# Kernel tuning notes

Hardware: AMD Instinct MI355X
Metric: run time of the kernel (lower is better)

The kernel has to match this reference:

```python
import jax, jax.numpy as jnp
import numpy as np

B, N, D = 8192, 8192, 768

def setup_inputs() -> dict:
    key = jax.random.key(0)
    kx, ky = jax.random.split(key)
    x = jax.random.normal(kx, (B, D), dtype=jnp.float32)
    y = jax.random.normal(ky, (N, D), dtype=jnp.float32)
    return {"x": x, "y": y}

def reference(x, y):
    # Pairwise squared L2 distances: ||x_i - y_j||^2 = ||x_i||^2 + ||y_j||^2 - 2 x_i . y_j
    # Mathematically identical to the naive broadcast (x[:,None,:]-y[None,:,:])**2 sum,
    # but avoids the O(B*N*D) intermediate. Clamp at 0 to guard fp cancellation
    # (true squared distances are nonnegative).
    x2 = jnp.sum(x * x, axis=-1)[:, None]           # [B, 1]
    y2 = jnp.sum(y * y, axis=-1)[None, :]           # [1, N]
    xy = jnp.einsum('bd,nd->bn', x, y)              # [B, N] GEMM
    d = x2 + y2 - 2.0 * xy
    return jnp.maximum(d, 0.0)
```

## Files before the change

kernel.cpp:

```cpp
#include <hip/hip_runtime.h>
#include <hip/hip_bf16.h>
#include <stdint.h>


#define M_DIM 8192
#define N_DIM 8192
#define D_DIM 768
#define K_DIM (3 * D_DIM)
#define BM 128
#define BN 128
#define BK 32

typedef __bf16 bf16x8 __attribute__((ext_vector_type(8)));
typedef float f32x4 __attribute__((ext_vector_type(4)));

#define GLOAD_LDS16(g, l) \
  __builtin_amdgcn_global_load_lds((const __attribute__((address_space(1))) void*)(g), \
                                   (__attribute__((address_space(3))) void*)(l), 16, 0, 0)

__global__ __launch_bounds__(256) void pack_kernel(
    const float* __restrict__ in, __hip_bfloat16* __restrict__ pk,
    float* __restrict__ nrm, int off_hi0, int off_hi1, int off_lo)
{
  int row = blockIdx.x;
  int tid = threadIdx.x;
  const float* r = in + (size_t)row * D_DIM;
  __hip_bfloat16* p = pk + (size_t)row * K_DIM;
  float ss = 0.f;
  for (int d = tid; d < D_DIM; d += 256) {
    float v = r[d];
    ss += v * v;
    __hip_bfloat16 hi = __float2bfloat16(v);
    float hv = __bfloat162float(hi);
    __hip_bfloat16 lo = __float2bfloat16(v - hv);
    p[off_hi0 + d] = hi;
    p[off_hi1 + d] = hi;
    p[off_lo  + d] = lo;
  }
  #pragma unroll
  for (int o = 32; o > 0; o >>= 1) ss += __shfl_down(ss, o, 64);
  __shared__ float warp_s[4];
  int lane = tid & 63, wid = tid >> 6;
  if (lane == 0) warp_s[wid] = ss;
  __syncthreads();
  if (tid == 0) nrm[row] = warp_s[0] + warp_s[1] + warp_s[2] + warp_s[3];
}

__global__ __launch_bounds__(256, 2) void dist_gemm(
    const __hip_bfloat16* __restrict__ A, const __hip_bfloat16* __restrict__ Bp,
    const float* __restrict__ x2, const float* __restrict__ y2,
    float* __restrict__ out)
{
  __shared__ __attribute__((aligned(16))) __hip_bfloat16 As[BM * BK];
  __shared__ __attribute__((aligned(16))) __hip_bfloat16 Bs[BN * BK];

  int bid = blockIdx.x;
  int swz = (bid & 7) * 512 + (bid >> 3);
  int tileRow = swz >> 6;
  int tileCol = swz & 63;
  int rowBase = tileRow * BM;
  int colBase = tileCol * BN;

  int tid  = threadIdx.x;
  int lane = tid & 63;
  int wid  = tid >> 6;
  int wr = wid >> 1, wc = wid & 1;

  f32x4 acc[4][4];
  #pragma unroll
  for (int m = 0; m < 4; ++m)
    #pragma unroll
    for (int n = 0; n < 4; ++n)
      acc[m][n] = (f32x4){0.f, 0.f, 0.f, 0.f};

  int reg0 = wid * 2;
  int kc = (lane >> 4) * 8;
  int rl = lane & 15;

  for (int kt = 0; kt < K_DIM / BK; ++kt) {
    int k0 = kt * BK;
    #pragma unroll
    for (int i = 0; i < 2; ++i) {
      int c = (reg0 + i) * 64 + lane;
      int arow = c >> 2;
      int cc = (c & 3) * 8;
      const __hip_bfloat16* ga = A  + (size_t)(rowBase + arow) * K_DIM + k0 + cc;
      const __hip_bfloat16* gb = Bp + (size_t)(colBase + arow) * K_DIM + k0 + cc;
      GLOAD_LDS16(ga, (char*)As + (reg0 + i) * 1024);
      GLOAD_LDS16(gb, (char*)Bs + (reg0 + i) * 1024);
    }
    __syncthreads();

    bf16x8 af[4], bfr[4];
    #pragma unroll
    for (int m = 0; m < 4; ++m)
      af[m] = *(const bf16x8*)&As[(wr * 64 + m * 16 + rl) * BK + kc];
    #pragma unroll
    for (int n = 0; n < 4; ++n)
      bfr[n] = *(const bf16x8*)&Bs[(wc * 64 + n * 16 + rl) * BK + kc];

    #pragma unroll
    for (int m = 0; m < 4; ++m)
      #pragma unroll
      for (int n = 0; n < 4; ++n)
        acc[m][n] = __builtin_amdgcn_mfma_f32_16x16x32_bf16(af[m], bfr[n], acc[m][n], 0, 0, 0);

    __syncthreads();
  }

  #pragma unroll
  for (int m = 0; m < 4; ++m) {
    int r0 = rowBase + wr * 64 + m * 16 + (lane >> 4) * 4;
    float4 xv = *(const float4*)&x2[r0];
    const float* xs = (const float*)&xv;
    #pragma unroll
    for (int n = 0; n < 4; ++n) {
      int c0 = colBase + wc * 64 + n * 16 + (lane & 15);
      float yv = y2[c0];
      float* op = out + (size_t)r0 * N_DIM + c0;
      #pragma unroll
      for (int v = 0; v < 4; ++v) {
        float d = xs[v] + yv - 2.0f * acc[m][n][v];
        op[(size_t)v * N_DIM] = fmaxf(d, 0.f);
      }
    }
  }
}

__global__ __launch_bounds__(256) void fallback_kernel(
    const float* __restrict__ x, const float* __restrict__ y, float* __restrict__ out)
{
  size_t gid = (size_t)blockIdx.x * 256 + threadIdx.x;
  int i = (int)(gid >> 13);
  int j = (int)(gid & 8191);
  const float4* xr = (const float4*)(x + (size_t)i * D_DIM);
  const float4* yr = (const float4*)(y + (size_t)j * D_DIM);
  float acc = 0.f;
  for (int d = 0; d < D_DIM / 4; ++d) {
    float4 a = xr[d], b = yr[d];
    float dx = a.x - b.x, dy = a.y - b.y, dz = a.z - b.z, dw = a.w - b.w;
    acc += dx * dx + dy * dy + dz * dz + dw * dw;
  }
  out[gid] = fmaxf(acc, 0.f);
}

extern "C" void kernel_launch(void* const* d_in, const int* in_sizes, int n_in,
                              void* d_out, int out_size, void* d_ws, size_t ws_size,
                              hipStream_t stream)
{
  const float* x = (const float*)d_in[0];
  const float* y = (const float*)d_in[1];
  float* out = (float*)d_out;

  size_t packBytes = (size_t)M_DIM * K_DIM * sizeof(__hip_bfloat16);
  size_t need = 2 * packBytes + 2 * (size_t)M_DIM * sizeof(float);
  if (ws_size < need) {
    fallback_kernel<<<((size_t)M_DIM * N_DIM) / 256, 256, 0, stream>>>(x, y, out);
    return;
  }

  __hip_bfloat16* Ap = (__hip_bfloat16*)d_ws;
  __hip_bfloat16* Bp = (__hip_bfloat16*)((char*)d_ws + packBytes);
  float* x2 = (float*)((char*)d_ws + 2 * packBytes);
  float* y2 = x2 + M_DIM;

  pack_kernel<<<M_DIM, 256, 0, stream>>>(x, Ap, x2, 0, D_DIM, 2 * D_DIM);
  pack_kernel<<<N_DIM, 256, 0, stream>>>(y, Bp, y2, 0, 2 * D_DIM, D_DIM);

  dist_gemm<<<(M_DIM / BM) * (N_DIM / BN), 256, 0, stream>>>(Ap, Bp, x2, y2, out);
}
```

Baseline: 694.5 us.

## Use 256x256 tiles with 4-stage LDS pipeline, swizzled LDS, vectorized pack

The GEMM now uses 256x256 output tiles with 512 threads, where each wave computes 128x64. Operand tiles stream through a 4-deep ring of LDS buffers filled by async global-to-LDS loads, with explicit vmcnt waits and one barrier per k-step in place of two syncthreads. The LDS layout is XOR-swizzled to cut bank conflicts, and MFMA issue is given raised priority. The pack kernel goes to one wave per row with 16-byte vector loads and stores, which raises LDS and register pressure in exchange for more reuse and overlap of loads with compute.

```diff
diff --git a/kernel.cpp b/kernel.cpp
--- a/kernel.cpp
+++ b/kernel.cpp
@@ -7,9 +7,10 @@
 #define N_DIM 8192
 #define D_DIM 768
 #define K_DIM (3 * D_DIM)
-#define BM 128
-#define BN 128
+#define BM 256
+#define BN 256
 #define BK 32
+#define KT (K_DIM / BK)
 
 typedef __bf16 bf16x8 __attribute__((ext_vector_type(8)));
 typedef float f32x4 __attribute__((ext_vector_type(4)));
@@ -22,95 +23,118 @@
     const float* __restrict__ in, __hip_bfloat16* __restrict__ pk,
     float* __restrict__ nrm, int off_hi0, int off_hi1, int off_lo)
 {
-  int row = blockIdx.x;
-  int tid = threadIdx.x;
+  int wid = threadIdx.x >> 6, lane = threadIdx.x & 63;
+  int row = blockIdx.x * 4 + wid;
   const float* r = in + (size_t)row * D_DIM;
   __hip_bfloat16* p = pk + (size_t)row * K_DIM;
   float ss = 0.f;
-  for (int d = tid; d < D_DIM; d += 256) {
-    float v = r[d];
-    ss += v * v;
-    __hip_bfloat16 hi = __float2bfloat16(v);
-    float hv = __bfloat162float(hi);
-    __hip_bfloat16 lo = __float2bfloat16(v - hv);
-    p[off_hi0 + d] = hi;
-    p[off_hi1 + d] = hi;
-    p[off_lo  + d] = lo;
-  }
+
+  auto proc = [&](int u) {
+    float4 a = *(const float4*)(r + u * 8);
+    float4 b = *(const float4*)(r + u * 8 + 4);
+    float v[8] = {a.x, a.y, a.z, a.w, b.x, b.y, b.z, b.w};
+    union { __hip_bfloat16 h[8]; uint4 q; } H, L;
+    #pragma unroll
+    for (int j = 0; j < 8; ++j) {
+      float x = v[j];
+      ss += x * x;
+      __hip_bfloat16 hi = __float2bfloat16(x);
+      H.h[j] = hi;
+      L.h[j] = __float2bfloat16(x - __bfloat162float(hi));
+    }
+    *(uint4*)(p + off_hi0 + u * 8) = H.q;
+    *(uint4*)(p + off_hi1 + u * 8) = H.q;
+    *(uint4*)(p + off_lo  + u * 8) = L.q;
+  };
+
+  proc(lane);
+  if (lane < 32) proc(64 + lane);
+
   #pragma unroll
-  for (int o = 32; o > 0; o >>= 1) ss += __shfl_down(ss, o, 64);
-  __shared__ float warp_s[4];
-  int lane = tid & 63, wid = tid >> 6;
-  if (lane == 0) warp_s[wid] = ss;
-  __syncthreads();
-  if (tid == 0) nrm[row] = warp_s[0] + warp_s[1] + warp_s[2] + warp_s[3];
+  for (int o = 1; o < 64; o <<= 1) ss += __shfl_xor(ss, o, 64);
+  if (lane == 0) nrm[row] = ss;
 }
 
-__global__ __launch_bounds__(256, 2) void dist_gemm(
+__global__ __launch_bounds__(512, 2) void dist_gemm(
     const __hip_bfloat16* __restrict__ A, const __hip_bfloat16* __restrict__ Bp,
     const float* __restrict__ x2, const float* __restrict__ y2,
     float* __restrict__ out)
 {
-  __shared__ __attribute__((aligned(16))) __hip_bfloat16 As[BM * BK];
-  __shared__ __attribute__((aligned(16))) __hip_bfloat16 Bs[BN * BK];
+  __shared__ __attribute__((aligned(16))) __hip_bfloat16 As[4][BM * BK];
+  __shared__ __attribute__((aligned(16))) __hip_bfloat16 Bs[4][BN * BK];
 
   int bid = blockIdx.x;
-  int swz = (bid & 7) * 512 + (bid >> 3);
-  int tileRow = swz >> 6;
-  int tileCol = swz & 63;
+  int swz = (bid & 7) * 128 + (bid >> 3);
+  int tileRow = swz >> 5;
+  int tileCol = swz & 31;
   int rowBase = tileRow * BM;
   int colBase = tileCol * BN;
 
   int tid  = threadIdx.x;
   int lane = tid & 63;
   int wid  = tid >> 6;
-  int wr = wid >> 1, wc = wid & 1;
+  int wr = wid >> 2, wc = wid & 3;
+  int rl = lane & 15, g = lane >> 4;
 
-  f32x4 acc[4][4];
+  auto STAGE = [&](int t) {
+    int b = t & 3;
+    int k0 = t * BK;
+    #pragma unroll
+    for (int s = 0; s < 2; ++s) {
+      int pby = (s * 512 + tid) * 16;
+      int o = pby ^ ((pby >> 2) & 48);
+      int row = o >> 6, colb = o & 63;
+      const __hip_bfloat16* ga = A  + (size_t)(rowBase + row) * K_DIM + k0 + (colb >> 1);
+      const __hip_bfloat16* gb = Bp + (size_t)(colBase + row) * K_DIM + k0 + (colb >> 1);
+      GLOAD_LDS16(ga, (char*)&As[b][0] + s * 8192 + wid * 1024);
+      GLOAD_LDS16(gb, (char*)&Bs[b][0] + s * 8192 + wid * 1024);
+    }
+  };
+
+  f32x4 acc[8][4];
   #pragma unroll
-  for (int m = 0; m < 4; ++m)
+  for (int m = 0; m < 8; ++m)
     #pragma unroll
     for (int n = 0; n < 4; ++n)
       acc[m][n] = (f32x4){0.f, 0.f, 0.f, 0.f};
 
-  int reg0 = wid * 2;
-  int kc = (lane >> 4) * 8;
-  int rl = lane & 15;
+  STAGE(0); STAGE(1); STAGE(2);
+  asm volatile("s_waitcnt vmcnt(8)" ::: "memory");
+  __builtin_amdgcn_s_barrier();
 
-  for (int kt = 0; kt < K_DIM / BK; ++kt) {
-    int k0 = kt * BK;
+  for (int kt = 0; kt < KT; ++kt) {
+    int b = kt & 3;
+    if (kt + 3 < KT) STAGE(kt + 3);
+
+    bf16x8 af[8], bf[4];
     #pragma unroll
-    for (int i = 0; i < 2; ++i) {
-      int c = (reg0 + i) * 64 + lane;
-      int arow = c >> 2;
-      int cc = (c & 3) * 8;
-      const __hip_bfloat16* ga = A  + (size_t)(rowBase + arow) * K_DIM + k0 + cc;
-      const __hip_bfloat16* gb = Bp + (size_t)(colBase + arow) * K_DIM + k0 + cc;
-      GLOAD_LDS16(ga, (char*)As + (reg0 + i) * 1024);
-      GLOAD_LDS16(gb, (char*)Bs + (reg0 + i) * 1024);
+    for (int m = 0; m < 8; ++m) {
+      int row = wr * 128 + m * 16 + rl;
+      af[m] = *(const bf16x8*)((const char*)&As[b][0] + (row << 6) + ((g << 4) ^ ((row & 3) << 4)));
     }
-    __syncthreads();
+    #pragma unroll
+    for (int n = 0; n < 4; ++n) {
+      int row = wc * 64 + n * 16 + rl;
+      bf[n] = *(const bf16x8*)((const char*)&Bs[b][0] + (row << 6) + ((g << 4) ^ ((row & 3) << 4)));
+    }
 
-    bf16x8 af[4], bfr[4];
+    __builtin_amdgcn_s_setprio(1);
     #pragma unroll
-    for (int m = 0; m < 4; ++m)
-      af[m] = *(const bf16x8*)&As[(wr * 64 + m * 16 + rl) * BK + kc];
-    #pragma unroll
-    for (int n = 0; n < 4; ++n)
-      bfr[n] = *(const bf16x8*)&Bs[(wc * 64 + n * 16 + rl) * BK + kc];
-
-    #pragma unroll
-    for (int m = 0; m < 4; ++m)
+    for (int m = 0; m < 8; ++m)
       #pragma unroll
       for (int n = 0; n < 4; ++n)
-        acc[m][n] = __builtin_amdgcn_mfma_f32_16x16x32_bf16(af[m], bfr[n], acc[m][n], 0, 0, 0);
+        acc[m][n] = __builtin_amdgcn_mfma_f32_16x16x32_bf16(af[m], bf[n], acc[m][n], 0, 0, 0);
+    __builtin_amdgcn_s_setprio(0);
 
-    __syncthreads();
+    if (kt < KT - 3)       asm volatile("s_waitcnt vmcnt(8)" ::: "memory");
+    else if (kt == KT - 3) asm volatile("s_waitcnt vmcnt(4)" ::: "memory");
+    else if (kt == KT - 2) asm volatile("s_waitcnt vmcnt(0)" ::: "memory");
+    if (kt < KT - 1) __builtin_amdgcn_s_barrier();
   }
 
   #pragma unroll
-  for (int m = 0; m < 4; ++m) {
-    int r0 = rowBase + wr * 64 + m * 16 + (lane >> 4) * 4;
+  for (int m = 0; m < 8; ++m) {
+    int r0 = rowBase + wr * 128 + m * 16 + (lane >> 4) * 4;
     float4 xv = *(const float4*)&x2[r0];
     const float* xs = (const float*)&xv;
     #pragma unroll
@@ -164,8 +188,8 @@
   float* x2 = (float*)((char*)d_ws + 2 * packBytes);
   float* y2 = x2 + M_DIM;
 
-  pack_kernel<<<M_DIM, 256, 0, stream>>>(x, Ap, x2, 0, D_DIM, 2 * D_DIM);
-  pack_kernel<<<N_DIM, 256, 0, stream>>>(y, Bp, y2, 0, 2 * D_DIM, D_DIM);
+  pack_kernel<<<M_DIM / 4, 256, 0, stream>>>(x, Ap, x2, 0, D_DIM, 2 * D_DIM);
+  pack_kernel<<<N_DIM / 4, 256, 0, stream>>>(y, Bp, y2, 0, 2 * D_DIM, D_DIM);
 
-  dist_gemm<<<(M_DIM / BM) * (N_DIM / BN), 256, 0, stream>>>(Ap, Bp, x2, y2, out);
+  dist_gemm<<<(M_DIM / BM) * (N_DIM / BN), 512, 0, stream>>>(Ap, Bp, x2, y2, out);
 }
```

New measurement: 680.6 us. 1.02x faster.
